# Optimization experiments

Hardware: AMD Instinct MI355X
Metric: run time of the kernel (lower is better)

The kernel has to match this reference:

```python
import jax, jax.numpy as jnp
import numpy as np
from jax import lax

WINDOW_SIZE = 11
GAUSSIAN_SIGMA = 1.5
C1 = (0.01 * 255.0) ** 2
C2 = (0.03 * 255.0) ** 2


def _gaussian_window(ws: int, sigma: float) -> np.ndarray:
    # matches cv2.getGaussianKernel(ws, sigma) outer-product window
    ax = np.arange(ws, dtype=np.float64) - (ws - 1) / 2.0
    g = np.exp(-(ax ** 2) / (2.0 * sigma ** 2))
    g = g / g.sum()
    return np.outer(g, g)  # [ws, ws], sums to 1


def _depthwise_conv(x, kernel):
    # x: [B, C, H, W]; kernel: [ws, ws] shared across channels (groups=C)
    c = x.shape[1]
    k = jnp.broadcast_to(kernel.astype(x.dtype)[None, None], (c, 1, kernel.shape[0], kernel.shape[1]))
    return lax.conv_general_dilated(
        x, k, window_strides=(1, 1), padding='VALID',
        dimension_numbers=('NCHW', 'OIHW', 'NCHW'),
        feature_group_count=c)


def setup_inputs() -> dict:
    key = jax.random.key(0)
    k1, k2 = jax.random.split(key)
    shape = (16, 3, 512, 512)
    raw_tensor = jax.random.uniform(k1, shape, dtype=jnp.float32)
    dst_tensor = jax.random.uniform(k2, shape, dtype=jnp.float32)
    return {"raw_tensor": raw_tensor, "dst_tensor": dst_tensor}


def reference(raw_tensor, dst_tensor):
    window = jnp.asarray(_gaussian_window(WINDOW_SIZE, GAUSSIAN_SIGMA), dtype=raw_tensor.dtype)
    raw = raw_tensor * 255.0
    dst = dst_tensor * 255.0

    raw_mean = _depthwise_conv(raw, window)
    dst_mean = _depthwise_conv(dst, window)
    raw_mean_sq = raw_mean ** 2
    dst_mean_sq = dst_mean ** 2
    raw_dst_mean = raw_mean * dst_mean

    raw_var = _depthwise_conv(raw * raw, window) - raw_mean_sq
    dst_var = _depthwise_conv(dst * dst, window) - dst_mean_sq
    raw_dst_cov = _depthwise_conv(raw * dst, window) - raw_dst_mean

    numer = (2.0 * raw_dst_mean + C1) * (2.0 * raw_dst_cov + C2)
    denom = (raw_mean_sq + dst_mean_sq + C1) * (raw_var + dst_var + C2)
    ssim_map = numer / denom  # [B, C, H-ws+1, W-ws+1]
    return jnp.mean(ssim_map, axis=(1, 2, 3))  # [B]
```

## Files before the change

kernel.cpp:

```cpp
#include <hip/hip_runtime.h>
#include <math.h>


#define WSZ 11
#define IMG 512
#define OSZ 502
#define NT  256
#define CH_OUT 32
#define NCHUNK 16
#define NSLOT 11
#define LA 6

struct WinArg { float w[WSZ]; };

typedef float f2 __attribute__((ext_vector_type(2)));
typedef float f4v __attribute__((ext_vector_type(4)));

typedef const __attribute__((address_space(1))) unsigned int* gp_t;
typedef __attribute__((address_space(3))) unsigned int* sp_t;

#define C1V 1.0e-4f
#define C2V 9.0e-4f

__device__ __forceinline__ void pkfma(f2& acc, f2 a, f2 b) {
    acc = __builtin_elementwise_fma(a, b, acc);
}

__global__ __launch_bounds__(NT, 3) void ssim_pk3(
    const float* __restrict__ rawp, const float* __restrict__ dstp,
    float* __restrict__ out, WinArg wa, float inv_n)
{
    __shared__ f4v srow[3344];
    __shared__ float wred[NT / 64];

    const int tid  = threadIdx.x;
    const int lane = tid & 63;
    const int wave = tid >> 6;
    const int chunk = blockIdx.x;
    const int img   = blockIdx.y;

    const int o0    = chunk * CH_OUT;
    const int olim  = min(o0 + CH_OUT, OSZ);
    const int rlast = min(o0 + CH_OUT + WSZ - 2, IMG - 1);
    const int NR    = rlast - o0 + 1;

    const bool w3     = (wave == 3);
    const int  nch    = w3 ? 4 : 5;
    const int  slotf4 = w3 ? 64 : 80;
    f4v* region = srow + wave * 880;
    const int  rl     = (w3 && lane > 58) ? 58 : lane;
    const bool active = !(w3 && lane > 58);

    const size_t ibase = (size_t)img * (size_t)(IMG * IMG);
    const float* lane_base = ((lane & 1) ? dstp : rawp) + ibase
                           + (size_t)(wave * 128 + (lane >> 1));

    f2 wv[WSZ];
#pragma unroll
    for (int j = 0; j < WSZ; ++j) { wv[j].x = wa.w[j]; wv[j].y = wa.w[j]; }

#define STAGE(ROW, SLOT)                                                       \
    {                                                                          \
        const float* _s = lane_base + (size_t)(ROW) * IMG;                     \
        float* _d = (float*)(region + (SLOT) * slotf4);                        \
        _Pragma("unroll")                                                      \
        for (int _c = 0; _c < 5; ++_c) {                                       \
            if (_c < nch)                                                      \
                __builtin_amdgcn_global_load_lds(                              \
                    (gp_t)(const void*)(_s + 32 * _c),                         \
                    (sp_t)(void*)(_d + 64 * _c), 4, 0, 0);                     \
        }                                                                      \
    }

    f2 hs12[WSZ][2];
    f2 hs34[WSZ][2];
    float acc = 0.0f;

#pragma unroll
    for (int r = 0; r < LA; ++r) STAGE(o0 + r, r)

#pragma unroll 1
    for (int rr = 0; rr < NR; rr += WSZ) {
#pragma unroll
        for (int k = 0; k < WSZ; ++k) {
            const int klin = rr + k;
            if (klin < NR) {
                {
                    int rs = klin + LA; if (rs > NR - 1) rs = NR - 1;
                    STAGE(o0 + rs, (k + LA) % NSLOT)
                }
                asm volatile("s_waitcnt vmcnt(24)" ::: "memory");

                f4v q[6];
                {
                    const f4v* rp = region + k * slotf4 + rl;
#pragma unroll
                    for (int j = 0; j < 6; ++j) q[j] = rp[j];
                }

                f2 s12a = {0.f, 0.f}, s34a = {0.f, 0.f};
                f2 s12b = {0.f, 0.f}, s34b = {0.f, 0.f};
#pragma unroll
                for (int e = 0; e < 12; ++e) {
                    const f2 rd = (e & 1) ? q[e >> 1].zw : q[e >> 1].xy;
                    const f2 rr2 = rd * rd;
                    f2 sp;
                    sp.x = rr2.x + rr2.y;
                    sp.y = rd.x * rd.y;
                    if (e < 11) {
                        pkfma(s12a, wv[e], rd);
                        pkfma(s34a, wv[e], sp);
                    }
                    if (e >= 1) {
                        pkfma(s12b, wv[e - 1], rd);
                        pkfma(s34b, wv[e - 1], sp);
                    }
                }
                hs12[k][0] = s12a; hs34[k][0] = s34a;
                hs12[k][1] = s12b; hs34[k][1] = s34b;

                const int o = o0 + klin - (WSZ - 1);
                if (klin >= WSZ - 1 && o < olim && active) {
                    f2 m12a = {0.f, 0.f}, m34a = {0.f, 0.f};
                    f2 m12b = {0.f, 0.f}, m34b = {0.f, 0.f};
#pragma unroll
                    for (int i = 0; i < WSZ; ++i) {
                        const int s = (k + 1 + i) % WSZ;
                        pkfma(m12a, wv[i], hs12[s][0]);
                        pkfma(m34a, wv[i], hs34[s][0]);
                        pkfma(m12b, wv[i], hs12[s][1]);
                        pkfma(m34b, wv[i], hs34[s][1]);
                    }
                    {
                        const float m1 = m12a.x, m2 = m12a.y;
                        const float m3 = m34a.x, m4 = m34a.y;
                        const float q1 = m1 * m1, q2 = m2 * m2, mm = m1 * m2;
                        const float num = (2.f * mm + C1V) * (2.f * (m4 - mm) + C2V);
                        const float den = (q1 + q2 + C1V) * (((m3 - q1) - q2) + C2V);
                        acc += num * __builtin_amdgcn_rcpf(den);
                    }
                    {
                        const float m1 = m12b.x, m2 = m12b.y;
                        const float m3 = m34b.x, m4 = m34b.y;
                        const float q1 = m1 * m1, q2 = m2 * m2, mm = m1 * m2;
                        const float num = (2.f * mm + C1V) * (2.f * (m4 - mm) + C2V);
                        const float den = (q1 + q2 + C1V) * (((m3 - q1) - q2) + C2V);
                        acc += num * __builtin_amdgcn_rcpf(den);
                    }
                }
            }
        }
    }
#undef STAGE

#pragma unroll
    for (int off = 32; off > 0; off >>= 1) acc += __shfl_down(acc, off, 64);
    if (lane == 0) wred[wave] = acc;
    __syncthreads();
    if (tid == 0) {
        const float tot = (wred[0] + wred[1]) + (wred[2] + wred[3]);
        atomicAdd(out + img / 3, tot * inv_n);
    }
}

extern "C" void kernel_launch(void* const* d_in, const int* in_sizes, int n_in,
                              void* d_out, int out_size, void* d_ws, size_t ws_size,
                              hipStream_t stream) {
    const float* raw = (const float*)d_in[0];
    const float* dst = (const float*)d_in[1];
    float* out = (float*)d_out;

    hipMemsetAsync(out, 0, (size_t)out_size * sizeof(float), stream);

    WinArg wa;
    double g[WSZ], s = 0.0;
    for (int i = 0; i < WSZ; ++i) {
        double ax = (double)i - (double)(WSZ - 1) / 2.0;
        g[i] = exp(-(ax * ax) / (2.0 * 1.5 * 1.5));
        s += g[i];
    }
    for (int i = 0; i < WSZ; ++i) wa.w[i] = (float)(g[i] / s);

    const float inv_n = (float)(1.0 / (3.0 * (double)OSZ * (double)OSZ));

    dim3 grid(NCHUNK, 48);
    ssim_pk3<<<grid, NT, 0, stream>>>(raw, dst, out, wa, inv_n);
}
```

Baseline: 59.39 us.

## Process two rows per step with a 12-slot ring and more ILP

The row loop now handles two input rows per iteration. It stages two rows ahead at once and loads both rows' LDS data before running their horizontal and vertical passes back to back. The LDS ring and history buffer grow from 11 to 12 slots so the two-row stepping wraps evenly, and the wait counts are adjusted per wave. Launch bounds drop from 3 to 2 blocks per CU, giving the compiler more registers for the doubled in-flight work at the cost of lower occupancy.

```diff
diff --git a/kernel.cpp b/kernel.cpp
--- a/kernel.cpp
+++ b/kernel.cpp
@@ -8,7 +8,7 @@
 #define NT  256
 #define CH_OUT 32
 #define NCHUNK 16
-#define NSLOT 11
+#define NS 12
 #define LA 6
 
 struct WinArg { float w[WSZ]; };
@@ -26,11 +26,11 @@
     acc = __builtin_elementwise_fma(a, b, acc);
 }
 
-__global__ __launch_bounds__(NT, 3) void ssim_pk3(
+__global__ __launch_bounds__(NT, 2) void ssim_ilp2(
     const float* __restrict__ rawp, const float* __restrict__ dstp,
     float* __restrict__ out, WinArg wa, float inv_n)
 {
-    __shared__ f4v srow[3344];
+    __shared__ f4v srow[3648];
     __shared__ float wred[NT / 64];
 
     const int tid  = threadIdx.x;
@@ -47,7 +47,7 @@
     const bool w3     = (wave == 3);
     const int  nch    = w3 ? 4 : 5;
     const int  slotf4 = w3 ? 64 : 80;
-    f4v* region = srow + wave * 880;
+    f4v* region = srow + wave * 960;
     const int  rl     = (w3 && lane > 58) ? 58 : lane;
     const bool active = !(w3 && lane > 58);
 
@@ -72,86 +72,99 @@
         }                                                                      \
     }
 
-    f2 hs12[WSZ][2];
-    f2 hs34[WSZ][2];
+#define HPASS(QQ, KS)                                                          \
+    {                                                                          \
+        f2 s12a = {0.f, 0.f}, s34a = {0.f, 0.f};                               \
+        f2 s12b = {0.f, 0.f}, s34b = {0.f, 0.f};                               \
+        _Pragma("unroll")                                                      \
+        for (int e = 0; e < 12; ++e) {                                         \
+            const f2 rd = (e & 1) ? QQ[e >> 1].zw : QQ[e >> 1].xy;             \
+            const f2 rr2 = rd * rd;                                            \
+            f2 sp;                                                             \
+            sp.x = rr2.x + rr2.y;                                              \
+            sp.y = rd.x * rd.y;                                                \
+            if (e < 11) { pkfma(s12a, wv[e], rd); pkfma(s34a, wv[e], sp); }    \
+            if (e >= 1) { pkfma(s12b, wv[e-1], rd); pkfma(s34b, wv[e-1], sp); }\
+        }                                                                      \
+        hs12[KS][0] = s12a; hs34[KS][0] = s34a;                                \
+        hs12[KS][1] = s12b; hs34[KS][1] = s34b;                                \
+    }
+
+#define VPASS(KOFF)                                                            \
+    {                                                                          \
+        f2 m12a = {0.f, 0.f}, m34a = {0.f, 0.f};                               \
+        f2 m12b = {0.f, 0.f}, m34b = {0.f, 0.f};                               \
+        _Pragma("unroll")                                                      \
+        for (int i = 0; i < WSZ; ++i) {                                        \
+            const int s = ((KOFF) + i) % NS;                                   \
+            pkfma(m12a, wv[i], hs12[s][0]);                                    \
+            pkfma(m34a, wv[i], hs34[s][0]);                                    \
+            pkfma(m12b, wv[i], hs12[s][1]);                                    \
+            pkfma(m34b, wv[i], hs34[s][1]);                                    \
+        }                                                                      \
+        {                                                                      \
+            const float m1 = m12a.x, m2 = m12a.y;                              \
+            const float m3 = m34a.x, m4 = m34a.y;                              \
+            const float q1 = m1 * m1, q2 = m2 * m2, mm = m1 * m2;              \
+            const float num = (2.f * mm + C1V) * (2.f * (m4 - mm) + C2V);      \
+            const float den = (q1 + q2 + C1V) * (((m3 - q1) - q2) + C2V);      \
+            acc += num * __builtin_amdgcn_rcpf(den);                           \
+        }                                                                      \
+        {                                                                      \
+            const float m1 = m12b.x, m2 = m12b.y;                              \
+            const float m3 = m34b.x, m4 = m34b.y;                              \
+            const float q1 = m1 * m1, q2 = m2 * m2, mm = m1 * m2;              \
+            const float num = (2.f * mm + C1V) * (2.f * (m4 - mm) + C2V);      \
+            const float den = (q1 + q2 + C1V) * (((m3 - q1) - q2) + C2V);      \
+            acc += num * __builtin_amdgcn_rcpf(den);                           \
+        }                                                                      \
+    }
+
+    f2 hs12[NS][2];
+    f2 hs34[NS][2];
     float acc = 0.0f;
 
 #pragma unroll
     for (int r = 0; r < LA; ++r) STAGE(o0 + r, r)
 
 #pragma unroll 1
-    for (int rr = 0; rr < NR; rr += WSZ) {
-#pragma unroll
-        for (int k = 0; k < WSZ; ++k) {
-            const int klin = rr + k;
+    for (int rr = 0; rr < NR; rr += NS) {
+#pragma unroll
+        for (int S = 0; S < NS / 2; ++S) {
+            const int klin = rr + 2 * S;
             if (klin < NR) {
                 {
-                    int rs = klin + LA; if (rs > NR - 1) rs = NR - 1;
-                    STAGE(o0 + rs, (k + LA) % NSLOT)
+                    int ra = klin + 6; if (ra > NR - 1) ra = NR - 1;
+                    int rb = klin + 7; if (rb > NR - 1) rb = NR - 1;
+                    STAGE(o0 + ra, (2 * S + 6) % NS)
+                    STAGE(o0 + rb, (2 * S + 7) % NS)
                 }
-                asm volatile("s_waitcnt vmcnt(24)" ::: "memory");
-
-                f4v q[6];
+                if (!w3) asm volatile("s_waitcnt vmcnt(30)" ::: "memory");
+                else     asm volatile("s_waitcnt vmcnt(24)" ::: "memory");
+
+                f4v q0[6], q1[6];
                 {
-                    const f4v* rp = region + k * slotf4 + rl;
-#pragma unroll
-                    for (int j = 0; j < 6; ++j) q[j] = rp[j];
+                    const f4v* rp0 = region + ((2 * S)     % NS) * slotf4 + rl;
+                    const f4v* rp1 = region + ((2 * S + 1) % NS) * slotf4 + rl;
+#pragma unroll
+                    for (int j = 0; j < 6; ++j) q0[j] = rp0[j];
+#pragma unroll
+                    for (int j = 0; j < 6; ++j) q1[j] = rp1[j];
                 }
 
-                f2 s12a = {0.f, 0.f}, s34a = {0.f, 0.f};
-                f2 s12b = {0.f, 0.f}, s34b = {0.f, 0.f};
-#pragma unroll
-                for (int e = 0; e < 12; ++e) {
-                    const f2 rd = (e & 1) ? q[e >> 1].zw : q[e >> 1].xy;
-                    const f2 rr2 = rd * rd;
-                    f2 sp;
-                    sp.x = rr2.x + rr2.y;
-                    sp.y = rd.x * rd.y;
-                    if (e < 11) {
-                        pkfma(s12a, wv[e], rd);
-                        pkfma(s34a, wv[e], sp);
-                    }
-                    if (e >= 1) {
-                        pkfma(s12b, wv[e - 1], rd);
-                        pkfma(s34b, wv[e - 1], sp);
-                    }
-                }
-                hs12[k][0] = s12a; hs34[k][0] = s34a;
-                hs12[k][1] = s12b; hs34[k][1] = s34b;
-
-                const int o = o0 + klin - (WSZ - 1);
-                if (klin >= WSZ - 1 && o < olim && active) {
-                    f2 m12a = {0.f, 0.f}, m34a = {0.f, 0.f};
-                    f2 m12b = {0.f, 0.f}, m34b = {0.f, 0.f};
-#pragma unroll
-                    for (int i = 0; i < WSZ; ++i) {
-                        const int s = (k + 1 + i) % WSZ;
-                        pkfma(m12a, wv[i], hs12[s][0]);
-                        pkfma(m34a, wv[i], hs34[s][0]);
-                        pkfma(m12b, wv[i], hs12[s][1]);
-                        pkfma(m34b, wv[i], hs34[s][1]);
-                    }
-                    {
-                        const float m1 = m12a.x, m2 = m12a.y;
-                        const float m3 = m34a.x, m4 = m34a.y;
-                        const float q1 = m1 * m1, q2 = m2 * m2, mm = m1 * m2;
-                        const float num = (2.f * mm + C1V) * (2.f * (m4 - mm) + C2V);
-                        const float den = (q1 + q2 + C1V) * (((m3 - q1) - q2) + C2V);
-                        acc += num * __builtin_amdgcn_rcpf(den);
-                    }
-                    {
-                        const float m1 = m12b.x, m2 = m12b.y;
-                        const float m3 = m34b.x, m4 = m34b.y;
-                        const float q1 = m1 * m1, q2 = m2 * m2, mm = m1 * m2;
-                        const float num = (2.f * mm + C1V) * (2.f * (m4 - mm) + C2V);
-                        const float den = (q1 + q2 + C1V) * (((m3 - q1) - q2) + C2V);
-                        acc += num * __builtin_amdgcn_rcpf(den);
-                    }
-                }
+                HPASS(q0, (2 * S) % NS)
+                if (klin >= WSZ - 1 && (o0 + klin - (WSZ - 1)) < olim && active)
+                    VPASS((2 * S + 2) % NS)
+
+                HPASS(q1, (2 * S + 1) % NS)
+                if (klin + 1 >= WSZ - 1 && (o0 + klin + 1 - (WSZ - 1)) < olim && active)
+                    VPASS((2 * S + 3) % NS)
             }
         }
     }
 #undef STAGE
+#undef HPASS
+#undef VPASS
 
 #pragma unroll
     for (int off = 32; off > 0; off >>= 1) acc += __shfl_down(acc, off, 64);
@@ -184,5 +197,5 @@
     const float inv_n = (float)(1.0 / (3.0 * (double)OSZ * (double)OSZ));
 
     dim3 grid(NCHUNK, 48);
-    ssim_pk3<<<grid, NT, 0, stream>>>(raw, dst, out, wa, inv_n);
+    ssim_ilp2<<<grid, NT, 0, stream>>>(raw, dst, out, wa, inv_n);
 }
```

Result: slower. 62.30 us (+4.9%).
